# Kernel tuning notes

Hardware: AMD Instinct MI355X
Metric: run time of the kernel (lower is better)

The kernel has to match this reference:

```python
import jax, jax.numpy as jnp
import numpy as np

HIDDEN = 2048
NH = 32        # query heads
NKV = 4        # kv heads
D = 128        # head dim
T = 2048       # tokens
WINDOW = 512   # sliding window
EPS = 1e-6
THETA = 1000000.0
SCALE = D ** -0.5


def setup_inputs() -> dict:
    key = jax.random.key(0)
    k1, k2, k3 = jax.random.split(key, 3)
    return {
        "positions": jnp.arange(T, dtype=jnp.int64) if jax.config.jax_enable_x64 else jnp.arange(T, dtype=jnp.int32),
        "hidden_states": jax.random.normal(k1, (T, HIDDEN), dtype=jnp.float32),
        "w_qkv": jax.random.normal(k2, (HIDDEN, (NH + 2 * NKV) * D), dtype=jnp.float32) * 0.02,
        "w_o": jax.random.normal(k3, (NH * D, HIDDEN), dtype=jnp.float32) * 0.02,
        "q_norm_w": jnp.ones((D,), dtype=jnp.float32),
        "k_norm_w": jnp.ones((D,), dtype=jnp.float32),
    }


def _rms_norm(x, w):
    # x: [..., D]; per-head RMSNorm
    var = jnp.mean(x * x, axis=-1, keepdims=True)
    return x * jax.lax.rsqrt(var + EPS) * w


def _rope(x, positions):
    # x: [T, H, D], neox-style rotary over full head dim
    inv_freq = 1.0 / (THETA ** (jnp.arange(0, D, 2, dtype=jnp.float32) / D))  # [D/2]
    freqs = positions.astype(jnp.float32)[:, None] * inv_freq                 # [T, D/2]
    cos = jnp.cos(freqs)[:, None, :]
    sin = jnp.sin(freqs)[:, None, :]
    x1, x2 = x[..., : D // 2], x[..., D // 2 :]
    return jnp.concatenate([x1 * cos - x2 * sin, x2 * cos + x1 * sin], axis=-1)


def reference(positions, hidden_states, w_qkv, w_o, q_norm_w, k_norm_w):
    qkv = hidden_states @ w_qkv                                   # [T, (NH+2NKV)*D]
    q, k, v = jnp.split(qkv, [NH * D, (NH + NKV) * D], axis=-1)
    q = _rms_norm(q.reshape(T, NH, D), q_norm_w)
    k = _rms_norm(k.reshape(T, NKV, D), k_norm_w)
    v = v.reshape(T, NKV, D)
    q = _rope(q, positions)
    k = _rope(k, positions)
    # GQA: expand kv heads to query heads
    rep = NH // NKV
    k = jnp.repeat(k, rep, axis=1)                                # [T, NH, D]
    v = jnp.repeat(v, rep, axis=1)
    scores = jnp.einsum("qhd,khd->hqk", q, k) * SCALE             # [NH, T, T]
    i = jnp.arange(T)[:, None]
    j = jnp.arange(T)[None, :]
    mask = (j <= i) & (i - j < WINDOW)                            # causal sliding window
    scores = jnp.where(mask[None, :, :], scores, jnp.finfo(scores.dtype).min)
    probs = jax.nn.softmax(scores, axis=-1)
    out = jnp.einsum("hqk,khd->qhd", probs, v).reshape(T, NH * D)
    return out @ w_o
```

## Files before the change

kernel.cpp:

```cpp
#include <hip/hip_runtime.h>
#include <math.h>

#define T      2048
#define HIDDEN 2048
#define NH     32
#define NKV    4
#define D      128
#define WINDOW 512
#define QKVW   ((NH + 2 * NKV) * D)
#define ODIM   (NH * D)
#define EPS    1e-6f
#define SCALE  0.08838834764831845f
#define PSTR   68
#define ESTR   136
#define VSTR   36
#define QMUL   ((float)(0.08838834764831845 * 1.4426950408889634))
#define MLOG2E 5.7707801635558536f

typedef _Float16 f16x8 __attribute__((ext_vector_type(8)));
typedef _Float16 f16x4 __attribute__((ext_vector_type(4)));
typedef float    f32x4 __attribute__((ext_vector_type(4)));


__device__ __forceinline__ void gl2lds16(const void* g, void* l) {
  __builtin_amdgcn_global_load_lds((const __attribute__((address_space(1))) void*)g,
                                   (__attribute__((address_space(3))) void*)l,
                                   16, 0, 0);
}

#define NB_A  2048
#define NB_B1 5120
#define NB_B2 4096
__global__ __launch_bounds__(256)
void prep(const float* __restrict__ hidden, const float* __restrict__ w_qkv,
          const float* __restrict__ w_o, const int* __restrict__ positions,
          _Float16* __restrict__ Ah1, _Float16* __restrict__ Bp1,
          _Float16* __restrict__ Bp2, float* __restrict__ cosT,
          float* __restrict__ sinT) {
  const int bx = blockIdx.x;
  const int tid = threadIdx.x;
  if (bx < NB_A) {
    const int cid = bx * 256 + tid;
    const int c = cid & 63;
    const int tile = cid >> 6;
    const int mtg = tile & (T / 16 - 1);
    const int kt = tile >> 7;
    const float* src = hidden + (size_t)(mtg * 16 + (c & 15)) * HIDDEN + kt * 32 + (c >> 4) * 8;
    const float4 a = *(const float4*)src;
    const float4 b = *(const float4*)(src + 4);
    f16x8 h;
    h[0] = (_Float16)a.x; h[1] = (_Float16)a.y; h[2] = (_Float16)a.z; h[3] = (_Float16)a.w;
    h[4] = (_Float16)b.x; h[5] = (_Float16)b.y; h[6] = (_Float16)b.z; h[7] = (_Float16)b.w;
    *(f16x8*)(Ah1 + (size_t)cid * 8) = h;
  } else if (bx < NB_A + NB_B1) {
    const int cid = (bx - NB_A) * 256 + tid;
    const int c = cid & 63;
    const int tile = cid >> 6;
    const int ntg = tile % (QKVW >> 4);
    const int kt = tile / (QKVW >> 4);
    const float* src = w_qkv + (size_t)(kt * 32 + (c >> 4) * 8) * QKVW + ntg * 16 + (c & 15);
    f16x8 h;
#pragma unroll
    for (int j = 0; j < 8; ++j) h[j] = (_Float16)src[(size_t)j * QKVW];
    *(f16x8*)(Bp1 + (size_t)cid * 8) = h;
  } else if (bx < NB_A + NB_B1 + NB_B2) {
    const int cid = (bx - NB_A - NB_B1) * 256 + tid;
    const int c = cid & 63;
    const int tile = cid >> 6;
    const int ntg = tile & (HIDDEN / 16 - 1);
    const int kt = tile >> 7;
    const float* src = w_o + (size_t)(kt * 32 + (c >> 4) * 8) * HIDDEN + ntg * 16 + (c & 15);
    f16x8 h;
#pragma unroll
    for (int j = 0; j < 8; ++j) h[j] = (_Float16)src[(size_t)j * HIDDEN];
    *(f16x8*)(Bp2 + (size_t)cid * 8) = h;
  } else {
    const int p0 = (bx - NB_A - NB_B1 - NB_B2) * 64 + (tid >> 6) * 16;
    const int j = tid & 63;
    const float invf = (float)pow(1.0e6, -(double)j / 64.0);
#pragma unroll 4
    for (int i = 0; i < 16; ++i) {
      const int t = p0 + i;
      const float ang = (float)positions[t] * invf;
      cosT[t * 64 + j] = cosf(ang);
      sinT[t * 64 + j] = sinf(ang);
    }
  }
}

#define KSTEPS 64

__global__ __launch_bounds__(256, 3)
void gemm_qkv(const _Float16* __restrict__ Apk, const _Float16* __restrict__ Bpk,
              const float* __restrict__ qnw, const float* __restrict__ knw,
              const float* __restrict__ cosT, const float* __restrict__ sinT,
              _Float16* __restrict__ Qpk, _Float16* __restrict__ Kpk,
              _Float16* __restrict__ Vpk) {
  extern __shared__ _Float16 SM[];
  const int tid = threadIdx.x;
  const int lane = tid & 63;
  const int wv = tid >> 6;
  const int l15 = lane & 15;
  const int l4 = lane >> 4;
  const int bx = blockIdx.x, by = blockIdx.y;

  f32x4 acc[2][8];
#pragma unroll
  for (int i = 0; i < 2; ++i)
#pragma unroll
    for (int j = 0; j < 8; ++j) acc[i][j] = (f32x4)0.f;

  auto stage = [&](int k, int s) {
    const int u = wv * 4 + s;
    char* dst = (char*)SM + (k % 3) * 16384 +
                (u < 8 ? u * 1024 : 8192 + (u - 8) * 1024);
    const char* src = (u < 8)
        ? (const char*)Apk + ((size_t)k * (T / 16) + by * 8 + u) * 1024 + lane * 16
        : (const char*)Bpk + ((size_t)k * (QKVW / 16) + bx * 8 + (u - 8)) * 1024 + lane * 16;
    gl2lds16(src, dst);
  };

#pragma unroll
  for (int k = 0; k < 2; ++k)
#pragma unroll
    for (int s = 0; s < 4; ++s) stage(k, s);
  asm volatile("s_waitcnt vmcnt(4)" ::: "memory");
  __builtin_amdgcn_s_barrier();
  __builtin_amdgcn_sched_barrier(0);

  int slot = 0;
  for (int t = 0; t < KSTEPS; ++t) {
    const _Float16* As = SM + slot * 8192;
    const _Float16* Bs = As + 4096;
    f16x8 af[2], bf[8];
#pragma unroll
    for (int i = 0; i < 2; ++i)
      af[i] = *(const f16x8*)(As + (wv * 2 + i) * 512 + lane * 8);
#pragma unroll
    for (int j = 0; j < 8; ++j)
      bf[j] = *(const f16x8*)(Bs + j * 512 + lane * 8);
    if (t + 2 < KSTEPS)
#pragma unroll
      for (int s = 0; s < 4; ++s) stage(t + 2, s);
    __builtin_amdgcn_s_setprio(1);
#pragma unroll
    for (int i = 0; i < 2; ++i)
#pragma unroll
      for (int j = 0; j < 8; ++j)
        acc[i][j] = __builtin_amdgcn_mfma_f32_16x16x32_f16(af[i], bf[j], acc[i][j], 0, 0, 0);
    __builtin_amdgcn_s_setprio(0);
    if (t < KSTEPS - 2)       asm volatile("s_waitcnt vmcnt(4)" ::: "memory");
    else if (t == KSTEPS - 2) asm volatile("s_waitcnt vmcnt(0)" ::: "memory");
    __builtin_amdgcn_s_barrier();
    __builtin_amdgcn_sched_barrier(0);
    slot = (slot == 2) ? 0 : slot + 1;
  }
  __syncthreads();

  if (bx < NH + NKV) {
    const bool isq = bx < NH;
    const float* w = isq ? qnw : knw;
    const float omul = isq ? QMUL : 1.0f;
    float wcol[8];
#pragma unroll
    for (int j = 0; j < 8; ++j) wcol[j] = w[j * 16 + l15];

    _Float16* ex = SM + wv * (32 * ESTR);
#pragma unroll
    for (int i = 0; i < 2; ++i)
#pragma unroll
      for (int r = 0; r < 4; ++r) {
        float ss = 0.f;
#pragma unroll
        for (int j = 0; j < 8; ++j) ss += acc[i][j][r] * acc[i][j][r];
        ss += __shfl_xor(ss, 1); ss += __shfl_xor(ss, 2);
        ss += __shfl_xor(ss, 4); ss += __shfl_xor(ss, 8);
        const float rn = 1.0f / sqrtf(ss * (1.0f / D) + EPS);
        const int row = i * 16 + l4 * 4 + r;
        const int t = by * 128 + wv * 32 + row;
#pragma unroll
        for (int j = 0; j < 4; ++j) {
          const int jc = j * 16 + l15;
          const float c = cosT[t * 64 + jc];
          const float s = sinT[t * 64 + jc];
          const float x1 = acc[i][j][r] * rn * wcol[j];
          const float x2 = acc[i][j + 4][r] * rn * wcol[j + 4];
          ex[row * ESTR + jc]      = (_Float16)((x1 * c - x2 * s) * omul);
          ex[row * ESTR + 64 + jc] = (_Float16)((x2 * c + x1 * s) * omul);
        }
      }
    const int hl = isq ? bx : bx - NH;
    _Float16* dst0 = isq ? Qpk : Kpk;
#pragma unroll
    for (int u = 0; u < 2; ++u) {
      const int qt = by * 8 + wv * 2 + u;
#pragma unroll
      for (int ds = 0; ds < 4; ++ds) {
        const f16x8 frag = *(const f16x8*)(ex + (u * 16 + l15) * ESTR + ds * 32 + l4 * 8);
        *(f16x8*)(dst0 + ((size_t)(hl * 128 + qt) * 4 + ds) * 512 + lane * 8) = frag;
      }
    }
  } else {
    const int kvh = bx - NH - NKV;
    _Float16* exv = SM + wv * (128 * VSTR);
#pragma unroll
    for (int i = 0; i < 2; ++i)
#pragma unroll
      for (int j = 0; j < 8; ++j) {
        f16x4 v4;
#pragma unroll
        for (int r = 0; r < 4; ++r) v4[r] = (_Float16)acc[i][j][r];
        *(f16x4*)(exv + (j * 16 + l15) * VSTR + i * 16 + l4 * 4) = v4;
      }
    const int kt64 = by * 2 + (wv >> 1);
    const int ks = wv & 1;
#pragma unroll
    for (int dt = 0; dt < 8; ++dt) {
      const f16x4 lo = *(const f16x4*)(exv + (dt * 16 + l15) * VSTR + l4 * 8);
      const f16x4 hi = *(const f16x4*)(exv + (dt * 16 + l15) * VSTR + l4 * 8 + 4);
      f16x8 h8;
#pragma unroll
      for (int r = 0; r < 4; ++r) { h8[r] = lo[r]; h8[r + 4] = hi[r]; }
      *(f16x8*)(Vpk + (((size_t)(kvh * 32 + kt64) * 2 + ks) * 8 + dt) * 512 + lane * 8) = h8;
    }
  }
}

template<int BN>
__global__ __launch_bounds__(256)
void gemm_f16(const _Float16* __restrict__ Apk, const _Float16* __restrict__ Bpk,
              float* __restrict__ C0, float* __restrict__ C1,
              int M, int N, int nkt) {
  constexpr int BM = 128;
  constexpr int AT = BM / 16;
  constexpr int BT = BN / 16;
  constexpr int RT = 4;
  constexpr int CT = BN / 32;
  __shared__ _Float16 As[2 * AT * 512];
  __shared__ _Float16 Bs[2 * BT * 512];

  const int tid = threadIdx.x;
  const int lane = tid & 63;
  const int wv = tid >> 6;
  const int wr = wv & 1, wc = wv >> 1;
  const int kt0 = blockIdx.z * nkt;
  float* __restrict__ C = blockIdx.z ? C1 : C0;

  f32x4 acc[RT][CT];
#pragma unroll
  for (int i = 0; i < RT; ++i)
#pragma unroll
    for (int j = 0; j < CT; ++j) acc[i][j] = (f32x4)0.f;

  const size_t Astep = (size_t)(M >> 4) * 1024;
  const size_t Bstep = (size_t)(N >> 4) * 1024;
  const char* Ag = (const char*)Apk + (size_t)kt0 * Astep +
                   (size_t)(blockIdx.y * AT) * 1024 + lane * 16;
  const char* Bg = (const char*)Bpk + (size_t)kt0 * Bstep +
                   (size_t)(blockIdx.x * BT) * 1024 + lane * 16;

  for (int kt2 = 0; kt2 < nkt; kt2 += 2) {
    const char* a0 = Ag + (size_t)kt2 * Astep;
    const char* b0 = Bg + (size_t)kt2 * Bstep;
#pragma unroll
    for (int t = wv; t < 2 * (AT + BT); t += 4) {
      const int half = t >= (AT + BT);
      const int tt = half ? t - (AT + BT) : t;
      if (tt < AT)
        gl2lds16(a0 + half * Astep + (size_t)tt * 1024,
                 (char*)As + (half * AT + tt) * 1024);
      else
        gl2lds16(b0 + half * Bstep + (size_t)(tt - AT) * 1024,
                 (char*)Bs + (half * BT + (tt - AT)) * 1024);
    }
    __syncthreads();

#pragma unroll
    for (int h2 = 0; h2 < 2; ++h2) {
      f16x8 af[RT], bf[CT];
#pragma unroll
      for (int i = 0; i < RT; ++i)
        af[i] = *(const f16x8*)((const char*)As + (h2 * AT + wr * RT + i) * 1024 + lane * 16);
#pragma unroll
      for (int j = 0; j < CT; ++j)
        bf[j] = *(const f16x8*)((const char*)Bs + (h2 * BT + wc * CT + j) * 1024 + lane * 16);
#pragma unroll
      for (int i = 0; i < RT; ++i)
#pragma unroll
        for (int j = 0; j < CT; ++j)
          acc[i][j] = __builtin_amdgcn_mfma_f32_16x16x32_f16(af[i], bf[j], acc[i][j], 0, 0, 0);
    }
    __syncthreads();
  }

  const int row0 = blockIdx.y * BM + wr * 64 + ((lane >> 4) << 2);
  const int col0 = blockIdx.x * BN + wc * (CT * 16) + (lane & 15);
#pragma unroll
  for (int i = 0; i < RT; ++i)
#pragma unroll
    for (int j = 0; j < CT; ++j) {
#pragma unroll
      for (int r = 0; r < 4; ++r)
        C[(size_t)(row0 + i * 16 + r) * N + col0 + j * 16] = acc[i][j][r];
    }
}

__global__ __launch_bounds__(256)
void reduce_add(const float4* __restrict__ a, const float4* __restrict__ b,
                float4* __restrict__ o, int n4) {
  for (int i = blockIdx.x * 256 + threadIdx.x; i < n4; i += gridDim.x * 256) {
    const float4 x = a[i], y = b[i];
    o[i] = make_float4(x.x + y.x, x.y + y.y, x.z + y.z, x.w + y.w);
  }
}

__global__ __launch_bounds__(256)
void attn_mfma(const _Float16* __restrict__ Qpk, const _Float16* __restrict__ Kpk,
               const _Float16* __restrict__ Vpk, _Float16* __restrict__ Ap2) {
  const int h = blockIdx.x;
  const int q0 = blockIdx.y * 128;
  const int kvh = h >> 3;
  const int tid = threadIdx.x;
  const int lane = tid & 63;
  const int wv = tid >> 6;
  const int l15 = lane & 15;
  const int l4 = lane >> 4;

  __shared__ _Float16 SM[8192 + 8192 + 4 * 32 * PSTR];
  _Float16* Ks = SM;
  _Float16* Vs = SM + 8192;
  _Float16* Pw = SM + 16384 + wv * 32 * PSTR;

  f16x8 qfA[4], qfB[4];
  {
    const _Float16* qa = Qpk + ((size_t)h * 128 + (q0 >> 4) + wv * 2) * 2048 + lane * 8;
#pragma unroll
    for (int ds = 0; ds < 4; ++ds) {
      qfA[ds] = *(const f16x8*)(qa + ds * 512);
      qfB[ds] = *(const f16x8*)(qa + 2048 + ds * 512);
    }
  }

  f16x8 ones;
#pragma unroll
  for (int j = 0; j < 8; ++j) ones[j] = (_Float16)1.0f;

  f32x4 OA[8], OB[8];
#pragma unroll
  for (int dt = 0; dt < 8; ++dt) { OA[dt] = (f32x4)0.f; OB[dt] = (f32x4)0.f; }
  f32x4 LA = (f32x4)0.f, LB = (f32x4)0.f;

  int kstart = q0 - (WINDOW - 1);
  if (kstart < 0) kstart = 0;
  kstart &= ~63;

  for (int kt = kstart; kt < q0 + 128; kt += 64) {
    __syncthreads();
    const _Float16* Kg = Kpk + ((size_t)kvh * 128 + (kt >> 4)) * 2048 + lane * 8;
    const _Float16* Vg = Vpk + ((size_t)kvh * 32 + (kt >> 6)) * 8192 + lane * 8;
#pragma unroll
    for (int t = wv; t < 16; t += 4) {
      gl2lds16(Kg + t * 512, (char*)Ks + t * 1024);
      gl2lds16(Vg + t * 512, (char*)Vs + t * 1024);
    }
    __syncthreads();

    f32x4 sA[4], sB[4];
#pragma unroll
    for (int nt = 0; nt < 4; ++nt) { sA[nt] = (f32x4)(-MLOG2E); sB[nt] = (f32x4)(-MLOG2E); }
#pragma unroll
    for (int ds = 0; ds < 4; ++ds) {
#pragma unroll
      for (int nt = 0; nt < 4; ++nt) {
        const f16x8 kf = *(const f16x8*)(Ks + (nt * 4 + ds) * 512 + lane * 8);
        sA[nt] = __builtin_amdgcn_mfma_f32_16x16x32_f16(qfA[ds], kf, sA[nt], 0, 0, 0);
        sB[nt] = __builtin_amdgcn_mfma_f32_16x16x32_f16(qfB[ds], kf, sB[nt], 0, 0, 0);
      }
    }

    const int qbA = q0 + wv * 32 + l4 * 4;
    const int kb = kt + l15;
#pragma unroll
    for (int nt = 0; nt < 4; ++nt) {
      const int kidx = kb + nt * 16;
#pragma unroll
      for (int r = 0; r < 4; ++r) {
        float pA = __builtin_amdgcn_exp2f(sA[nt][r]);
        float pB = __builtin_amdgcn_exp2f(sB[nt][r]);
        pA = ((unsigned)(qbA + r - kidx) < WINDOW) ? pA : 0.f;
        pB = ((unsigned)(qbA + 16 + r - kidx) < WINDOW) ? pB : 0.f;
        Pw[(l4 * 4 + r) * PSTR + nt * 16 + l15] = (_Float16)pA;
        Pw[(16 + l4 * 4 + r) * PSTR + nt * 16 + l15] = (_Float16)pB;
      }
    }

#pragma unroll
    for (int ks = 0; ks < 2; ++ks) {
      const f16x8 pfA = *(const f16x8*)(Pw + l15 * PSTR + ks * 32 + l4 * 8);
      const f16x8 pfB = *(const f16x8*)(Pw + (16 + l15) * PSTR + ks * 32 + l4 * 8);
      LA = __builtin_amdgcn_mfma_f32_16x16x32_f16(pfA, ones, LA, 0, 0, 0);
      LB = __builtin_amdgcn_mfma_f32_16x16x32_f16(pfB, ones, LB, 0, 0, 0);
#pragma unroll
      for (int dt = 0; dt < 8; ++dt) {
        const f16x8 vf = *(const f16x8*)(Vs + (ks * 8 + dt) * 512 + lane * 8);
        OA[dt] = __builtin_amdgcn_mfma_f32_16x16x32_f16(pfA, vf, OA[dt], 0, 0, 0);
        OB[dt] = __builtin_amdgcn_mfma_f32_16x16x32_f16(pfB, vf, OB[dt], 0, 0, 0);
      }
    }
  }

  __syncthreads();
  _Float16* Tw = SM + wv * 16 * ESTR;
#pragma unroll
  for (int half = 0; half < 2; ++half) {
    const f32x4* O = half ? OB : OA;
    const f32x4  L = half ? LB : LA;
    float inv[4];
#pragma unroll
    for (int r = 0; r < 4; ++r) inv[r] = 1.0f / L[r];
#pragma unroll
    for (int dt = 0; dt < 8; ++dt)
#pragma unroll
      for (int r = 0; r < 4; ++r)
        Tw[(l4 * 4 + r) * ESTR + dt * 16 + l15] = (_Float16)(O[dt][r] * inv[r]);
    const int qt = (q0 >> 4) + wv * 2 + half;
#pragma unroll
    for (int ds = 0; ds < 4; ++ds) {
      const f16x8 frag = *(const f16x8*)(Tw + l15 * ESTR + ds * 32 + l4 * 8);
      *(f16x8*)(Ap2 + ((size_t)(h * 4 + ds) * 128 + qt) * 512 + lane * 8) = frag;
    }
  }
}

extern "C" void kernel_launch(void* const* d_in, const int* in_sizes, int n_in,
                              void* d_out, int out_size, void* d_ws, size_t ws_size,
                              hipStream_t stream) {
  const int*   positions = (const int*)d_in[0];
  const float* hidden    = (const float*)d_in[1];
  const float* w_qkv     = (const float*)d_in[2];
  const float* w_o       = (const float*)d_in[3];
  const float* q_norm_w  = (const float*)d_in[4];
  const float* k_norm_w  = (const float*)d_in[5];
  float* out = (float*)d_out;

  char* ws = (char*)d_ws;
  _Float16* Kpk = (_Float16*)ws;
  _Float16* Vpk = Kpk + (size_t)T * NKV * D;
  ws += (size_t)T * QKVW * 4;
  _Float16* Ap2 = (_Float16*)ws;
  float* P0 = (float*)(ws + (size_t)T * ODIM * 2);
  ws += (size_t)T * ODIM * 4;
  float* cosT = (float*)ws;  ws += (size_t)T * 64 * 4;
  float* sinT = (float*)ws;  ws += (size_t)T * 64 * 4;
  _Float16* Bp1 = (_Float16*)ws; ws += (size_t)HIDDEN * QKVW * 2;
  _Float16* Bp2 = (_Float16*)ws; ws += (size_t)ODIM * HIDDEN * 2;
  _Float16* Ah1 = (_Float16*)ws; ws += (size_t)T * HIDDEN * 2;
  _Float16* Qpk = (_Float16*)ws;
  float* P1 = (float*)Qpk;
  ws += (size_t)T * ODIM * 2;

  prep<<<dim3(NB_A + NB_B1 + NB_B2 + T / 64), 256, 0, stream>>>(
      hidden, w_qkv, w_o, positions, Ah1, Bp1, Bp2, cosT, sinT);

  gemm_qkv<<<dim3(QKVW / 128, T / 128), 256, 49152, stream>>>(
      Ah1, Bp1, q_norm_w, k_norm_w, cosT, sinT, Qpk, Kpk, Vpk);

  attn_mfma<<<dim3(NH, T / 128), 256, 0, stream>>>(Qpk, Kpk, Vpk, Ap2);

  gemm_f16<128><<<dim3(HIDDEN / 128, T / 128, 2), 256, 0, stream>>>(
      Ap2, Bp2, P0, P1, T, HIDDEN, ODIM / 32 / 2);
  reduce_add<<<dim3(512), 256, 0, stream>>>((const float4*)P0, (const float4*)P1,
                                            (float4*)out, T * HIDDEN / 4);
}
```

Measured before the change: 290.3 us.

## Pipeline output-projection GEMM with triple-buffered LDS and add MFMA priority hints

Replaces the output-projection GEMM's synchronous double-k-step loads with a three-slot LDS ring buffer. Loads are issued two k-steps ahead and gated with explicit vmcnt waits and one barrier per step, so global-to-LDS copies overlap MFMA work. It also raises wave priority around MFMA blocks in both the GEMM and attention kernels, sets launch bounds for three blocks per CU, and doubles the reduce grid. The cost is 48KB of dynamic shared memory per block and hand-managed wait counts that depend on a fixed number of outstanding loads per wave.

```diff
diff --git a/kernel.cpp b/kernel.cpp
--- a/kernel.cpp
+++ b/kernel.cpp
@@ -226,19 +226,11 @@
   }
 }
 
-template<int BN>
-__global__ __launch_bounds__(256)
-void gemm_f16(const _Float16* __restrict__ Apk, const _Float16* __restrict__ Bpk,
-              float* __restrict__ C0, float* __restrict__ C1,
-              int M, int N, int nkt) {
-  constexpr int BM = 128;
-  constexpr int AT = BM / 16;
-  constexpr int BT = BN / 16;
-  constexpr int RT = 4;
-  constexpr int CT = BN / 32;
-  __shared__ _Float16 As[2 * AT * 512];
-  __shared__ _Float16 Bs[2 * BT * 512];
-
+__global__ __launch_bounds__(256, 3)
+void gemm_f16p(const _Float16* __restrict__ Apk, const _Float16* __restrict__ Bpk,
+               float* __restrict__ C0, float* __restrict__ C1,
+               int M, int N, int nkt) {
+  extern __shared__ _Float16 SM[];
   const int tid = threadIdx.x;
   const int lane = tid & 63;
   const int wv = tid >> 6;
@@ -246,59 +238,70 @@
   const int kt0 = blockIdx.z * nkt;
   float* __restrict__ C = blockIdx.z ? C1 : C0;
 
-  f32x4 acc[RT][CT];
-#pragma unroll
-  for (int i = 0; i < RT; ++i)
-#pragma unroll
-    for (int j = 0; j < CT; ++j) acc[i][j] = (f32x4)0.f;
+  f32x4 acc[4][4];
+#pragma unroll
+  for (int i = 0; i < 4; ++i)
+#pragma unroll
+    for (int j = 0; j < 4; ++j) acc[i][j] = (f32x4)0.f;
 
   const size_t Astep = (size_t)(M >> 4) * 1024;
   const size_t Bstep = (size_t)(N >> 4) * 1024;
   const char* Ag = (const char*)Apk + (size_t)kt0 * Astep +
-                   (size_t)(blockIdx.y * AT) * 1024 + lane * 16;
+                   (size_t)(blockIdx.y * 8) * 1024 + lane * 16;
   const char* Bg = (const char*)Bpk + (size_t)kt0 * Bstep +
-                   (size_t)(blockIdx.x * BT) * 1024 + lane * 16;
-
-  for (int kt2 = 0; kt2 < nkt; kt2 += 2) {
-    const char* a0 = Ag + (size_t)kt2 * Astep;
-    const char* b0 = Bg + (size_t)kt2 * Bstep;
-#pragma unroll
-    for (int t = wv; t < 2 * (AT + BT); t += 4) {
-      const int half = t >= (AT + BT);
-      const int tt = half ? t - (AT + BT) : t;
-      if (tt < AT)
-        gl2lds16(a0 + half * Astep + (size_t)tt * 1024,
-                 (char*)As + (half * AT + tt) * 1024);
-      else
-        gl2lds16(b0 + half * Bstep + (size_t)(tt - AT) * 1024,
-                 (char*)Bs + (half * BT + (tt - AT)) * 1024);
-    }
-    __syncthreads();
-
-#pragma unroll
-    for (int h2 = 0; h2 < 2; ++h2) {
-      f16x8 af[RT], bf[CT];
-#pragma unroll
-      for (int i = 0; i < RT; ++i)
-        af[i] = *(const f16x8*)((const char*)As + (h2 * AT + wr * RT + i) * 1024 + lane * 16);
-#pragma unroll
-      for (int j = 0; j < CT; ++j)
-        bf[j] = *(const f16x8*)((const char*)Bs + (h2 * BT + wc * CT + j) * 1024 + lane * 16);
-#pragma unroll
-      for (int i = 0; i < RT; ++i)
-#pragma unroll
-        for (int j = 0; j < CT; ++j)
-          acc[i][j] = __builtin_amdgcn_mfma_f32_16x16x32_f16(af[i], bf[j], acc[i][j], 0, 0, 0);
-    }
-    __syncthreads();
-  }
-
-  const int row0 = blockIdx.y * BM + wr * 64 + ((lane >> 4) << 2);
-  const int col0 = blockIdx.x * BN + wc * (CT * 16) + (lane & 15);
-#pragma unroll
-  for (int i = 0; i < RT; ++i)
-#pragma unroll
-    for (int j = 0; j < CT; ++j) {
+                   (size_t)(blockIdx.x * 8) * 1024 + lane * 16;
+
+  auto stage = [&](int k, int s) {
+    const int u = wv * 4 + s;
+    char* dst = (char*)SM + (k % 3) * 16384 +
+                (u < 8 ? u * 1024 : 8192 + (u - 8) * 1024);
+    const char* src = (u < 8) ? Ag + (size_t)k * Astep + u * 1024
+                              : Bg + (size_t)k * Bstep + (u - 8) * 1024;
+    gl2lds16(src, dst);
+  };
+
+#pragma unroll
+  for (int k = 0; k < 2; ++k)
+#pragma unroll
+    for (int s = 0; s < 4; ++s) stage(k, s);
+  asm volatile("s_waitcnt vmcnt(4)" ::: "memory");
+  __builtin_amdgcn_s_barrier();
+  __builtin_amdgcn_sched_barrier(0);
+
+  int slot = 0;
+  for (int t = 0; t < nkt; ++t) {
+    const _Float16* As = SM + slot * 8192;
+    const _Float16* Bs = As + 4096;
+    f16x8 af[4], bf[4];
+#pragma unroll
+    for (int i = 0; i < 4; ++i)
+      af[i] = *(const f16x8*)(As + (wr * 4 + i) * 512 + lane * 8);
+#pragma unroll
+    for (int j = 0; j < 4; ++j)
+      bf[j] = *(const f16x8*)(Bs + (wc * 4 + j) * 512 + lane * 8);
+    if (t + 2 < nkt)
+#pragma unroll
+      for (int s = 0; s < 4; ++s) stage(t + 2, s);
+    __builtin_amdgcn_s_setprio(1);
+#pragma unroll
+    for (int i = 0; i < 4; ++i)
+#pragma unroll
+      for (int j = 0; j < 4; ++j)
+        acc[i][j] = __builtin_amdgcn_mfma_f32_16x16x32_f16(af[i], bf[j], acc[i][j], 0, 0, 0);
+    __builtin_amdgcn_s_setprio(0);
+    if (t < nkt - 2)       asm volatile("s_waitcnt vmcnt(4)" ::: "memory");
+    else if (t == nkt - 2) asm volatile("s_waitcnt vmcnt(0)" ::: "memory");
+    __builtin_amdgcn_s_barrier();
+    __builtin_amdgcn_sched_barrier(0);
+    slot = (slot == 2) ? 0 : slot + 1;
+  }
+
+  const int row0 = blockIdx.y * 128 + wr * 64 + ((lane >> 4) << 2);
+  const int col0 = blockIdx.x * 128 + wc * 64 + (lane & 15);
+#pragma unroll
+  for (int i = 0; i < 4; ++i)
+#pragma unroll
+    for (int j = 0; j < 4; ++j) {
 #pragma unroll
       for (int r = 0; r < 4; ++r)
         C[(size_t)(row0 + i * 16 + r) * N + col0 + j * 16] = acc[i][j][r];
@@ -368,6 +371,7 @@
     f32x4 sA[4], sB[4];
 #pragma unroll
     for (int nt = 0; nt < 4; ++nt) { sA[nt] = (f32x4)(-MLOG2E); sB[nt] = (f32x4)(-MLOG2E); }
+    __builtin_amdgcn_s_setprio(1);
 #pragma unroll
     for (int ds = 0; ds < 4; ++ds) {
 #pragma unroll
@@ -377,6 +381,7 @@
         sB[nt] = __builtin_amdgcn_mfma_f32_16x16x32_f16(qfB[ds], kf, sB[nt], 0, 0, 0);
       }
     }
+    __builtin_amdgcn_s_setprio(0);
 
     const int qbA = q0 + wv * 32 + l4 * 4;
     const int kb = kt + l15;
@@ -394,6 +399,7 @@
       }
     }
 
+    __builtin_amdgcn_s_setprio(1);
 #pragma unroll
     for (int ks = 0; ks < 2; ++ks) {
       const f16x8 pfA = *(const f16x8*)(Pw + l15 * PSTR + ks * 32 + l4 * 8);
@@ -407,6 +413,7 @@
         OB[dt] = __builtin_amdgcn_mfma_f32_16x16x32_f16(pfB, vf, OB[dt], 0, 0, 0);
       }
     }
+    __builtin_amdgcn_s_setprio(0);
   }
 
   __syncthreads();
@@ -467,8 +474,8 @@
 
   attn_mfma<<<dim3(NH, T / 128), 256, 0, stream>>>(Qpk, Kpk, Vpk, Ap2);
 
-  gemm_f16<128><<<dim3(HIDDEN / 128, T / 128, 2), 256, 0, stream>>>(
+  gemm_f16p<<<dim3(HIDDEN / 128, T / 128, 2), 256, 49152, stream>>>(
       Ap2, Bp2, P0, P1, T, HIDDEN, ODIM / 32 / 2);
-  reduce_add<<<dim3(512), 256, 0, stream>>>((const float4*)P0, (const float4*)P1,
-                                            (float4*)out, T * HIDDEN / 4);
-}
+  reduce_add<<<dim3(1024), 256, 0, stream>>>((const float4*)P0, (const float4*)P1,
+                                             (float4*)out, T * HIDDEN / 4);
+}
```

Measured after the change: 276.3 us. 1.05x faster.
